# Kernel tuning notes

Measured on AMD Instinct MI355X. Metric: run time of the kernel, lower is better.

## Reference

```python
import jax, jax.numpy as jnp
import numpy as np

BN_EPS = 1e-5
CLUSTER_SIZE = 32  # K (real clusters kept after softmax)


def setup_inputs() -> dict:
    key = jax.random.key(0)
    ks = jax.random.split(key, 7)
    B, N, D, Ktot, K = 4096, 128, 512, 48, 32
    x = jax.random.normal(ks[0], (B, N, D), dtype=jnp.float32)
    clusters = jax.random.normal(ks[1], (D, Ktot), dtype=jnp.float32) / np.sqrt(D)
    bn_w = jax.random.uniform(ks[2], (Ktot,), dtype=jnp.float32)
    bn_b = jax.random.normal(ks[3], (Ktot,), dtype=jnp.float32)
    bn_rm = jax.random.normal(ks[4], (Ktot,), dtype=jnp.float32)
    bn_rv = jax.random.uniform(ks[5], (Ktot,), dtype=jnp.float32)  # positive variance
    clusters2 = jax.random.normal(ks[6], (1, D, K), dtype=jnp.float32) / np.sqrt(D)
    return {"x": x, "clusters": clusters, "bn_w": bn_w, "bn_b": bn_b,
            "bn_rm": bn_rm, "bn_rv": bn_rv, "clusters2": clusters2}


def reference(x, clusters, bn_w, bn_b, bn_rm, bn_rv, clusters2):
    # x: [B, N, D]; clusters: [D, Ktot]; clusters2: [1, D, K]
    B, N, D = x.shape
    K = clusters2.shape[-1]
    # cluster projection: [B, N, Ktot]
    logits = jnp.einsum('bnd,dk->bnk', x, clusters)
    # inference BatchNorm1d (affine with running stats)
    inv_std = jax.lax.rsqrt(bn_rv + BN_EPS)
    logits = (logits - bn_rm) * inv_std * bn_w + bn_b
    # softmax over real + ghost clusters, then drop ghost (no renorm)
    assignment = jax.nn.softmax(logits, axis=-1)[..., :K]  # [B, N, K]
    a_sum = jnp.sum(assignment, axis=1, keepdims=True)      # [B, 1, K]
    a = a_sum * clusters2                                   # [B, D, K]
    # weighted VLAD accumulate: [B, D, K]
    vlad = jnp.einsum('bnk,bnd->bdk', assignment, x) - a
    # intra-normalize (L2 across descriptor dim D, per cluster)
    vlad = vlad / jnp.maximum(jnp.linalg.norm(vlad, axis=1, keepdims=True), 1e-12)
    # flatten and L2-normalize full vector
    vlad = vlad.reshape(B, D * K)
    vlad = vlad / jnp.maximum(jnp.linalg.norm(vlad, axis=1, keepdims=True), 1e-12)
    return vlad
```

## Files before the change

### kernel.cpp

```cpp
#include <hip/hip_runtime.h>

typedef unsigned short u16;
typedef unsigned int u32;
typedef __attribute__((ext_vector_type(8))) short short8;
typedef __attribute__((ext_vector_type(4))) float f32x4;
typedef __attribute__((ext_vector_type(4))) u32 u32x4;

#define NPT 128
#define DIM 512
#define KT 48
#define KC 32
#define BPB 16

__device__ __forceinline__ u16 f2bf(float f) {
    unsigned u = __builtin_bit_cast(unsigned, f);
    return (u16)((u + 0x7FFFu + ((u >> 16) & 1u)) >> 16);
}

__device__ __forceinline__ u32 cvtpk(float lo, float hi) {
    u32 r;
    asm("v_cvt_pk_bf16_f32 %0, %1, %2" : "=v"(r) : "v"(lo), "v"(hi));
    return r;
}

__device__ __forceinline__ void lds_barrier() {
    asm volatile("s_waitcnt lgkmcnt(0)" ::: "memory");
    __builtin_amdgcn_s_barrier();
}

__device__ __forceinline__ int swz(int n) {
    return ((n & 7) ^ (((n >> 3) & 1) << 2)) << 4;
}

__global__ void prep_kernel(const float* __restrict__ clusters,
                            const float* __restrict__ bn_w,
                            const float* __restrict__ bn_b,
                            const float* __restrict__ bn_rm,
                            const float* __restrict__ bn_rv,
                            u16* __restrict__ cTs,
                            float* __restrict__ tvec) {
    const int k = blockIdx.x;
    const float s = bn_w[k] * rsqrtf(bn_rv[k] + 1e-5f);
    if (threadIdx.x == 0) tvec[k] = bn_b[k] - bn_rm[k] * s;
    for (int d = threadIdx.x; d < DIM; d += blockDim.x)
        cTs[k * DIM + d] = f2bf(clusters[d * KT + k] * s);
}

__global__ __launch_bounds__(512)
void vlad_kernel(const float* __restrict__ x,
                 const float* __restrict__ c2,
                 const u16* __restrict__ cTs,
                 const float* __restrict__ tvec,
                 float* __restrict__ out) {
    __shared__ __align__(16) u16 cTsL[KT * DIM];
    __shared__ __align__(16) u16 buf[2][16 * DIM];
    __shared__ __align__(16) u16 aT[KC][136];
    __shared__ float asum_part[8][KC];
    __shared__ float colsq_part[8][KC];

    const int tid  = threadIdx.x;
    const int wave = tid >> 6;
    const int lane = tid & 63;
    const int lr   = lane & 15;
    const int lg   = lane >> 4;

    const int b0i = blockIdx.x * BPB;
    const float* xblk = x + (size_t)b0i * (NPT * DIM);

    const float t0 = tvec[lr], t1 = tvec[16 + lr], t2 = tvec[32 + lr];

    const int srow = tid >> 5;
    const int scol = (tid & 31) * 16;
    const int sbyte = scol * 2;
    const int ssw = swz(srow);

    #pragma unroll
    for (int i = 0; i < 6; ++i) {
        int idx = tid + i * 512;
        int k = idx >> 6, slot = idx & 63;
        u32x4 v = *(const u32x4*)(cTs + k * DIM + slot * 8);
        *(u32x4*)((char*)cTsL + k * 1024 + ((slot * 16) ^ swz(k))) = v;
    }
    {
        const float* g = xblk + srow * DIM + scol;
        f32x4 a0 = *(const f32x4*)(g);
        f32x4 a1 = *(const f32x4*)(g + 4);
        f32x4 a2 = *(const f32x4*)(g + 8);
        f32x4 a3 = *(const f32x4*)(g + 12);
        u32x4 wA, wB;
        wA[0] = cvtpk(a0[0], a0[1]); wA[1] = cvtpk(a0[2], a0[3]);
        wA[2] = cvtpk(a1[0], a1[1]); wA[3] = cvtpk(a1[2], a1[3]);
        wB[0] = cvtpk(a2[0], a2[1]); wB[1] = cvtpk(a2[2], a2[3]);
        wB[2] = cvtpk(a3[0], a3[1]); wB[3] = cvtpk(a3[2], a3[3]);
        char* dst = (char*)buf[0] + srow * 1024;
        *(u32x4*)(dst + (sbyte ^ ssw)) = wA;
        *(u32x4*)(dst + ((sbyte + 16) ^ ssw)) = wB;
    }
    __syncthreads();

    for (int m = 0; m < BPB; ++m) {
        f32x4 acc0 = {0.f,0.f,0.f,0.f}, acc1 = {0.f,0.f,0.f,0.f}, acc2 = {0.f,0.f,0.f,0.f};
        short8 af2[4][4];

        #pragma unroll
        for (int ns = 0; ns < 4; ++ns) {
            #pragma unroll
            for (int h = 0; h < 2; ++h) {
                const int j = ns * 2 + h;
                const int cur = j & 1;
                const int gnext = m * 8 + j + 1;
                const bool pOK = (gnext < BPB * 8);

                f32x4 a0, a1, a2, a3;
                if (pOK) {
                    const float* g = xblk + (size_t)gnext * (16 * DIM) + srow * DIM + scol;
                    a0 = *(const f32x4*)(g);
                    a1 = *(const f32x4*)(g + 4);
                    a2 = *(const f32x4*)(g + 8);
                    a3 = *(const f32x4*)(g + 12);
                }

                if ((lane >> 5) == h) {
                    const int nb = (lg & 1) * 8;
                    #pragma unroll
                    for (int dti = 0; dti < 4; ++dti) {
                        const int dd = wave * 128 + dti * 32 + 2 * lr;
                        short8 v;
                        #pragma unroll
                        for (int jj = 0; jj < 8; ++jj) {
                            const int rr = nb + jj;
                            v[jj] = *(const short*)((const char*)buf[cur] + rr * 1024 + (dd ^ swz(rr)));
                        }
                        af2[ns][dti] = v;
                    }
                }

                if (wave == j) {
                    const char* xb = (const char*)buf[cur] + lr * 1024;
                    const int sw = swz(lr);
                    const char* c0 = (const char*)cTsL + lr * 1024;
                    const char* c1 = (const char*)cTsL + (16 + lr) * 1024;
                    const char* c2p = (const char*)cTsL + (32 + lr) * 1024;
                    const int s1 = swz(16 + lr), s2 = swz(32 + lr);
                    #pragma unroll 2
                    for (int step = 0; step < 16; ++step) {
                        const int off = step * 64 + lg * 16;
                        short8 af  = *(const short8*)(xb + (off ^ sw));
                        short8 bb0 = *(const short8*)(c0 + (off ^ sw));
                        short8 bb1 = *(const short8*)(c1 + (off ^ s1));
                        short8 bb2 = *(const short8*)(c2p + (off ^ s2));
                        acc0 = __builtin_amdgcn_mfma_f32_16x16x32_bf16(af, bb0, acc0, 0, 0, 0);
                        acc1 = __builtin_amdgcn_mfma_f32_16x16x32_bf16(af, bb1, acc1, 0, 0, 0);
                        acc2 = __builtin_amdgcn_mfma_f32_16x16x32_bf16(af, bb2, acc2, 0, 0, 0);
                    }
                }

                if (pOK) {
                    u32x4 wA, wB;
                    wA[0] = cvtpk(a0[0], a0[1]); wA[1] = cvtpk(a0[2], a0[3]);
                    wA[2] = cvtpk(a1[0], a1[1]); wA[3] = cvtpk(a1[2], a1[3]);
                    wB[0] = cvtpk(a2[0], a2[1]); wB[1] = cvtpk(a2[2], a2[3]);
                    wB[2] = cvtpk(a3[0], a3[1]); wB[3] = cvtpk(a3[2], a3[3]);
                    char* dst = (char*)buf[cur ^ 1] + srow * 1024;
                    *(u32x4*)(dst + (sbyte ^ ssw)) = wA;
                    *(u32x4*)(dst + ((sbyte + 16) ^ ssw)) = wB;
                }
                lds_barrier();
            }
        }

        {
            float a0[4], a1[4];
            #pragma unroll
            for (int r = 0; r < 4; ++r) {
                float l0 = acc0[r] + t0, l1 = acc1[r] + t1, l2 = acc2[r] + t2;
                float mx = fmaxf(fmaxf(l0, l1), l2);
                #pragma unroll
                for (int o = 1; o < 16; o <<= 1) mx = fmaxf(mx, __shfl_xor(mx, o));
                float e0 = __expf(l0 - mx), e1 = __expf(l1 - mx), e2 = __expf(l2 - mx);
                float s = e0 + e1 + e2;
                #pragma unroll
                for (int o = 1; o < 16; o <<= 1) s += __shfl_xor(s, o);
                float inv = 1.0f / s;
                a0[r] = e0 * inv; a1[r] = e1 * inv;
            }
            float p0 = 0.f, p1 = 0.f;
            #pragma unroll
            for (int r = 0; r < 4; ++r) {
                int n = wave * 16 + lg * 4 + r;
                aT[lr][n]      = f2bf(a0[r]);
                aT[16 + lr][n] = f2bf(a1[r]);
                p0 += a0[r]; p1 += a1[r];
            }
            p0 += __shfl_xor(p0, 16); p0 += __shfl_xor(p0, 32);
            p1 += __shfl_xor(p1, 16); p1 += __shfl_xor(p1, 32);
            if (lane < 16) { asum_part[wave][lane] = p0; asum_part[wave][16 + lane] = p1; }
        }
        lds_barrier();

        f32x4 vacc[4][2];
        #pragma unroll
        for (int i = 0; i < 4; ++i) {
            vacc[i][0] = (f32x4){0.f,0.f,0.f,0.f};
            vacc[i][1] = (f32x4){0.f,0.f,0.f,0.f};
        }
        #pragma unroll
        for (int ns = 0; ns < 4; ++ns) {
            short8 bf0 = *(const short8*)(&aT[lr][ns * 32 + lg * 8]);
            short8 bf1 = *(const short8*)(&aT[16 + lr][ns * 32 + lg * 8]);
            #pragma unroll
            for (int dti = 0; dti < 4; ++dti) {
                vacc[dti][0] = __builtin_amdgcn_mfma_f32_16x16x32_bf16(af2[ns][dti], bf0, vacc[dti][0], 0, 0, 0);
                vacc[dti][1] = __builtin_amdgcn_mfma_f32_16x16x32_bf16(af2[ns][dti], bf1, vacc[dti][1], 0, 0, 0);
            }
        }

        float as0 = 0.f, as1 = 0.f;
        #pragma unroll
        for (int w2 = 0; w2 < 8; ++w2) {
            as0 += asum_part[w2][lr];
            as1 += asum_part[w2][16 + lr];
        }
        float cs0 = 0.f, cs1 = 0.f;
        #pragma unroll
        for (int dti = 0; dti < 4; ++dti) {
            #pragma unroll
            for (int r = 0; r < 4; ++r) {
                int d = (wave * 4 + dti) * 16 + lg * 4 + r;
                float v0 = vacc[dti][0][r] - as0 * c2[d * KC + lr];
                float v1 = vacc[dti][1][r] - as1 * c2[d * KC + 16 + lr];
                vacc[dti][0][r] = v0; vacc[dti][1][r] = v1;
                cs0 += v0 * v0; cs1 += v1 * v1;
            }
        }
        cs0 += __shfl_xor(cs0, 16); cs0 += __shfl_xor(cs0, 32);
        cs1 += __shfl_xor(cs1, 16); cs1 += __shfl_xor(cs1, 32);
        if (lane < 16) { colsq_part[wave][lane] = cs0; colsq_part[wave][16 + lane] = cs1; }
        lds_barrier();
        float sq0 = 0.f, sq1 = 0.f;
        #pragma unroll
        for (int w2 = 0; w2 < 8; ++w2) {
            sq0 += colsq_part[w2][lr];
            sq1 += colsq_part[w2][16 + lr];
        }
        float cn0 = sqrtf(sq0), cn1 = sqrtf(sq1);
        float s10 = 1.0f / fmaxf(cn0, 1e-12f);
        float s11 = 1.0f / fmaxf(cn1, 1e-12f);
        float c10 = cn0 * s10, c11 = cn1 * s11;
        float tot = c10 * c10 + c11 * c11;
        #pragma unroll
        for (int o = 1; o < 16; o <<= 1) tot += __shfl_xor(tot, o);
        float gs = 1.0f / fmaxf(sqrtf(tot), 1e-12f);
        float sk0 = s10 * gs, sk1 = s11 * gs;
        {
            float* ob = out + (size_t)(b0i + m) * (DIM * KC);
            #pragma unroll
            for (int dti = 0; dti < 4; ++dti) {
                #pragma unroll
                for (int r = 0; r < 4; ++r) {
                    int d = (wave * 4 + dti) * 16 + lg * 4 + r;
                    ob[d * KC + lr]      = vacc[dti][0][r] * sk0;
                    ob[d * KC + 16 + lr] = vacc[dti][1][r] * sk1;
                }
            }
        }
    }
}

extern "C" void kernel_launch(void* const* d_in, const int* in_sizes, int n_in,
                              void* d_out, int out_size, void* d_ws, size_t ws_size,
                              hipStream_t stream) {
    const float* x        = (const float*)d_in[0];
    const float* clusters = (const float*)d_in[1];
    const float* bn_w     = (const float*)d_in[2];
    const float* bn_b     = (const float*)d_in[3];
    const float* bn_rm    = (const float*)d_in[4];
    const float* bn_rv    = (const float*)d_in[5];
    const float* c2       = (const float*)d_in[6];
    float* out = (float*)d_out;

    u16*   cTs  = (u16*)d_ws;
    float* tvec = (float*)((char*)d_ws + KT * DIM * sizeof(u16));

    const int B = in_sizes[0] / (NPT * DIM);

    prep_kernel<<<KT, 256, 0, stream>>>(clusters, bn_w, bn_b, bn_rm, bn_rv, cTs, tvec);
    vlad_kernel<<<B / BPB, 512, 0, stream>>>(x, c2, cTs, tvec, out);
}
```

Baseline: 368.7 us.

## Stream x chunks directly into LDS as fp32 via global_load_lds

Replaces the register-staged load, bf16 convert and LDS store of each 16-row x chunk with asynchronous global_load_lds DMA of raw fp32 into a double-buffered LDS tile. The bf16 conversion moves to the consumers: the MFMA wave converts its A fragments after reading, and the transposed fragment gather converts after reading. The aim is to take the global-to-register round trip and its VGPR pressure off the critical path. The cost is a doubled LDS footprint for the x buffers, which may reduce occupancy, plus extra conversion and scalar LDS reads per consumer.

New measurement: 395.8 us. +7.3%, slower.

```diff
diff --git a/kernel.cpp b/kernel.cpp
--- a/kernel.cpp
+++ b/kernel.cpp
@@ -11,6 +11,7 @@
 #define KT 48
 #define KC 32
 #define BPB 16
+#define NCH (BPB * 8)
 
 __device__ __forceinline__ u16 f2bf(float f) {
     unsigned u = __builtin_bit_cast(unsigned, f);
@@ -25,6 +26,11 @@
 
 __device__ __forceinline__ void lds_barrier() {
     asm volatile("s_waitcnt lgkmcnt(0)" ::: "memory");
+    __builtin_amdgcn_s_barrier();
+}
+
+__device__ __forceinline__ void chunk_barrier() {
+    asm volatile("s_waitcnt vmcnt(0) lgkmcnt(0)" ::: "memory");
     __builtin_amdgcn_s_barrier();
 }
 
@@ -46,14 +52,30 @@
         cTs[k * DIM + d] = f2bf(clusters[d * KT + k] * s);
 }
 
+#define CH_ISSUE(c)                                                          \
+    do {                                                                     \
+        const float* gc_ = xblk + (size_t)(c) * (16 * DIM);                  \
+        float* lb_ = &bufF[(c) & 1][0];                                      \
+        _Pragma("unroll")                                                    \
+        for (int i_ = 0; i_ < 4; ++i_) {                                     \
+            const int slot_ = wave * 4 + i_;                                 \
+            const int r_ = slot_ >> 1, half_ = slot_ & 1;                    \
+            const int us_ = (half_ * 64 + lane) ^ (r_ & 7);                  \
+            __builtin_amdgcn_global_load_lds(                                \
+                (const __attribute__((address_space(1))) u32*)(gc_ + r_ * DIM + us_ * 4), \
+                (__attribute__((address_space(3))) u32*)(lb_ + slot_ * 256), \
+                16, 0, 0);                                                   \
+        }                                                                    \
+    } while (0)
+
 __global__ __launch_bounds__(512)
 void vlad_kernel(const float* __restrict__ x,
                  const float* __restrict__ c2,
                  const u16* __restrict__ cTs,
                  const float* __restrict__ tvec,
                  float* __restrict__ out) {
+    __shared__ __align__(16) float bufF[2][16 * DIM];
     __shared__ __align__(16) u16 cTsL[KT * DIM];
-    __shared__ __align__(16) u16 buf[2][16 * DIM];
     __shared__ __align__(16) u16 aT[KC][136];
     __shared__ float asum_part[8][KC];
     __shared__ float colsq_part[8][KC];
@@ -68,11 +90,6 @@
     const float* xblk = x + (size_t)b0i * (NPT * DIM);
 
     const float t0 = tvec[lr], t1 = tvec[16 + lr], t2 = tvec[32 + lr];
-
-    const int srow = tid >> 5;
-    const int scol = (tid & 31) * 16;
-    const int sbyte = scol * 2;
-    const int ssw = swz(srow);
 
     #pragma unroll
     for (int i = 0; i < 6; ++i) {
@@ -81,22 +98,7 @@
         u32x4 v = *(const u32x4*)(cTs + k * DIM + slot * 8);
         *(u32x4*)((char*)cTsL + k * 1024 + ((slot * 16) ^ swz(k))) = v;
     }
-    {
-        const float* g = xblk + srow * DIM + scol;
-        f32x4 a0 = *(const f32x4*)(g);
-        f32x4 a1 = *(const f32x4*)(g + 4);
-        f32x4 a2 = *(const f32x4*)(g + 8);
-        f32x4 a3 = *(const f32x4*)(g + 12);
-        u32x4 wA, wB;
-        wA[0] = cvtpk(a0[0], a0[1]); wA[1] = cvtpk(a0[2], a0[3]);
-        wA[2] = cvtpk(a1[0], a1[1]); wA[3] = cvtpk(a1[2], a1[3]);
-        wB[0] = cvtpk(a2[0], a2[1]); wB[1] = cvtpk(a2[2], a2[3]);
-        wB[2] = cvtpk(a3[0], a3[1]); wB[3] = cvtpk(a3[2], a3[3]);
-        char* dst = (char*)buf[0] + srow * 1024;
-        *(u32x4*)(dst + (sbyte ^ ssw)) = wA;
-        *(u32x4*)(dst + ((sbyte + 16) ^ ssw)) = wB;
-    }
-    __syncthreads();
+    CH_ISSUE(0);
 
     for (int m = 0; m < BPB; ++m) {
         f32x4 acc0 = {0.f,0.f,0.f,0.f}, acc1 = {0.f,0.f,0.f,0.f}, acc2 = {0.f,0.f,0.f,0.f};
@@ -107,65 +109,57 @@
             #pragma unroll
             for (int h = 0; h < 2; ++h) {
                 const int j = ns * 2 + h;
-                const int cur = j & 1;
-                const int gnext = m * 8 + j + 1;
-                const bool pOK = (gnext < BPB * 8);
-
-                f32x4 a0, a1, a2, a3;
-                if (pOK) {
-                    const float* g = xblk + (size_t)gnext * (16 * DIM) + srow * DIM + scol;
-                    a0 = *(const f32x4*)(g);
-                    a1 = *(const f32x4*)(g + 4);
-                    a2 = *(const f32x4*)(g + 8);
-                    a3 = *(const f32x4*)(g + 12);
-                }
+                const int g = m * 8 + j;
+
+                chunk_barrier();
+                if (g + 1 < NCH) { CH_ISSUE(g + 1); }
+
+                const float* bcur = &bufF[j & 1][0];
 
                 if ((lane >> 5) == h) {
                     const int nb = (lg & 1) * 8;
                     #pragma unroll
                     for (int dti = 0; dti < 4; ++dti) {
-                        const int dd = wave * 128 + dti * 32 + 2 * lr;
-                        short8 v;
+                        const int d = wave * 64 + dti * 16 + lr;
+                        const int u = d >> 2, o = d & 3;
+                        float f[8];
                         #pragma unroll
                         for (int jj = 0; jj < 8; ++jj) {
                             const int rr = nb + jj;
-                            v[jj] = *(const short*)((const char*)buf[cur] + rr * 1024 + (dd ^ swz(rr)));
+                            f[jj] = bcur[rr * DIM + ((u ^ (rr & 7)) * 4 + o)];
                         }
-                        af2[ns][dti] = v;
+                        u32x4 w;
+                        w[0] = cvtpk(f[0], f[1]); w[1] = cvtpk(f[2], f[3]);
+                        w[2] = cvtpk(f[4], f[5]); w[3] = cvtpk(f[6], f[7]);
+                        af2[ns][dti] = __builtin_bit_cast(short8, w);
                     }
                 }
 
                 if (wave == j) {
-                    const char* xb = (const char*)buf[cur] + lr * 1024;
-                    const int sw = swz(lr);
-                    const char* c0 = (const char*)cTsL + lr * 1024;
-                    const char* c1 = (const char*)cTsL + (16 + lr) * 1024;
-                    const char* c2p = (const char*)cTsL + (32 + lr) * 1024;
-                    const int s1 = swz(16 + lr), s2 = swz(32 + lr);
-                    #pragma unroll 2
+                    const float* xrow = bcur + lr * DIM;
+                    const int xsw = lr & 7;
+                    const char* cb0 = (const char*)cTsL + lr * 1024;
+                    const char* cb1 = (const char*)cTsL + (16 + lr) * 1024;
+                    const char* cb2 = (const char*)cTsL + (32 + lr) * 1024;
+                    const int s0 = swz(lr), s1 = swz(16 + lr), s2 = swz(32 + lr);
+                    #pragma unroll 4
                     for (int step = 0; step < 16; ++step) {
+                        const int u0 = step * 8 + lg * 2;
+                        f32x4 xa = *(const f32x4*)(xrow + (u0 ^ xsw) * 4);
+                        f32x4 xb = *(const f32x4*)(xrow + ((u0 + 1) ^ xsw) * 4);
+                        u32x4 aw;
+                        aw[0] = cvtpk(xa[0], xa[1]); aw[1] = cvtpk(xa[2], xa[3]);
+                        aw[2] = cvtpk(xb[0], xb[1]); aw[3] = cvtpk(xb[2], xb[3]);
+                        short8 af = __builtin_bit_cast(short8, aw);
                         const int off = step * 64 + lg * 16;
-                        short8 af  = *(const short8*)(xb + (off ^ sw));
-                        short8 bb0 = *(const short8*)(c0 + (off ^ sw));
-                        short8 bb1 = *(const short8*)(c1 + (off ^ s1));
-                        short8 bb2 = *(const short8*)(c2p + (off ^ s2));
+                        short8 bb0 = *(const short8*)(cb0 + (off ^ s0));
+                        short8 bb1 = *(const short8*)(cb1 + (off ^ s1));
+                        short8 bb2 = *(const short8*)(cb2 + (off ^ s2));
                         acc0 = __builtin_amdgcn_mfma_f32_16x16x32_bf16(af, bb0, acc0, 0, 0, 0);
                         acc1 = __builtin_amdgcn_mfma_f32_16x16x32_bf16(af, bb1, acc1, 0, 0, 0);
                         acc2 = __builtin_amdgcn_mfma_f32_16x16x32_bf16(af, bb2, acc2, 0, 0, 0);
                     }
                 }
-
-                if (pOK) {
-                    u32x4 wA, wB;
-                    wA[0] = cvtpk(a0[0], a0[1]); wA[1] = cvtpk(a0[2], a0[3]);
-                    wA[2] = cvtpk(a1[0], a1[1]); wA[3] = cvtpk(a1[2], a1[3]);
-                    wB[0] = cvtpk(a2[0], a2[1]); wB[1] = cvtpk(a2[2], a2[3]);
-                    wB[2] = cvtpk(a3[0], a3[1]); wB[3] = cvtpk(a3[2], a3[3]);
-                    char* dst = (char*)buf[cur ^ 1] + srow * 1024;
-                    *(u32x4*)(dst + (sbyte ^ ssw)) = wA;
-                    *(u32x4*)(dst + ((sbyte + 16) ^ ssw)) = wB;
-                }
-                lds_barrier();
             }
         }
 
```

## Drop LDS cluster staging, interleave softmax and VLAD MFMAs, raise occupancy

Applied to the files above, without the earlier changes.

Removes the 48KB shared-memory copy of the scaled cluster matrix and reads the B operand directly from global memory (cache). The softmax and assignment write now happen inside each wave's logits stage, and the VLAD MFMA for each 32-point slice runs incrementally as slices complete. This cuts af2 register storage from 16 to 4 fragments. Batches per block are halved and launch bounds request 4 waves per SIMD, aiming for higher occupancy. In exchange the cluster operands come from global memory every step, and the smaller batch count doubles the per-block setup and prologue cost.

New measurement: 1.048 ms. 2.84x slower.

```diff
diff --git a/kernel.cpp b/kernel.cpp
--- a/kernel.cpp
+++ b/kernel.cpp
@@ -10,7 +10,7 @@
 #define DIM 512
 #define KT 48
 #define KC 32
-#define BPB 16
+#define BPB 8
 
 __device__ __forceinline__ u16 f2bf(float f) {
     unsigned u = __builtin_bit_cast(unsigned, f);
@@ -46,13 +46,12 @@
         cTs[k * DIM + d] = f2bf(clusters[d * KT + k] * s);
 }
 
-__global__ __launch_bounds__(512)
+__global__ __launch_bounds__(512, 4)
 void vlad_kernel(const float* __restrict__ x,
                  const float* __restrict__ c2,
                  const u16* __restrict__ cTs,
                  const float* __restrict__ tvec,
                  float* __restrict__ out) {
-    __shared__ __align__(16) u16 cTsL[KT * DIM];
     __shared__ __align__(16) u16 buf[2][16 * DIM];
     __shared__ __align__(16) u16 aT[KC][136];
     __shared__ float asum_part[8][KC];
@@ -74,13 +73,6 @@
     const int sbyte = scol * 2;
     const int ssw = swz(srow);
 
-    #pragma unroll
-    for (int i = 0; i < 6; ++i) {
-        int idx = tid + i * 512;
-        int k = idx >> 6, slot = idx & 63;
-        u32x4 v = *(const u32x4*)(cTs + k * DIM + slot * 8);
-        *(u32x4*)((char*)cTsL + k * 1024 + ((slot * 16) ^ swz(k))) = v;
-    }
     {
         const float* g = xblk + srow * DIM + scol;
         f32x4 a0 = *(const f32x4*)(g);
@@ -99,119 +91,118 @@
     __syncthreads();
 
     for (int m = 0; m < BPB; ++m) {
-        f32x4 acc0 = {0.f,0.f,0.f,0.f}, acc1 = {0.f,0.f,0.f,0.f}, acc2 = {0.f,0.f,0.f,0.f};
-        short8 af2[4][4];
-
-        #pragma unroll
-        for (int ns = 0; ns < 4; ++ns) {
-            #pragma unroll
-            for (int h = 0; h < 2; ++h) {
-                const int j = ns * 2 + h;
-                const int cur = j & 1;
-                const int gnext = m * 8 + j + 1;
-                const bool pOK = (gnext < BPB * 8);
-
-                f32x4 a0, a1, a2, a3;
-                if (pOK) {
-                    const float* g = xblk + (size_t)gnext * (16 * DIM) + srow * DIM + scol;
-                    a0 = *(const f32x4*)(g);
-                    a1 = *(const f32x4*)(g + 4);
-                    a2 = *(const f32x4*)(g + 8);
-                    a3 = *(const f32x4*)(g + 12);
-                }
-
-                if ((lane >> 5) == h) {
-                    const int nb = (lg & 1) * 8;
-                    #pragma unroll
-                    for (int dti = 0; dti < 4; ++dti) {
-                        const int dd = wave * 128 + dti * 32 + 2 * lr;
-                        short8 v;
-                        #pragma unroll
-                        for (int jj = 0; jj < 8; ++jj) {
-                            const int rr = nb + jj;
-                            v[jj] = *(const short*)((const char*)buf[cur] + rr * 1024 + (dd ^ swz(rr)));
-                        }
-                        af2[ns][dti] = v;
-                    }
-                }
-
-                if (wave == j) {
-                    const char* xb = (const char*)buf[cur] + lr * 1024;
-                    const int sw = swz(lr);
-                    const char* c0 = (const char*)cTsL + lr * 1024;
-                    const char* c1 = (const char*)cTsL + (16 + lr) * 1024;
-                    const char* c2p = (const char*)cTsL + (32 + lr) * 1024;
-                    const int s1 = swz(16 + lr), s2 = swz(32 + lr);
-                    #pragma unroll 2
-                    for (int step = 0; step < 16; ++step) {
-                        const int off = step * 64 + lg * 16;
-                        short8 af  = *(const short8*)(xb + (off ^ sw));
-                        short8 bb0 = *(const short8*)(c0 + (off ^ sw));
-                        short8 bb1 = *(const short8*)(c1 + (off ^ s1));
-                        short8 bb2 = *(const short8*)(c2p + (off ^ s2));
-                        acc0 = __builtin_amdgcn_mfma_f32_16x16x32_bf16(af, bb0, acc0, 0, 0, 0);
-                        acc1 = __builtin_amdgcn_mfma_f32_16x16x32_bf16(af, bb1, acc1, 0, 0, 0);
-                        acc2 = __builtin_amdgcn_mfma_f32_16x16x32_bf16(af, bb2, acc2, 0, 0, 0);
-                    }
-                }
-
-                if (pOK) {
-                    u32x4 wA, wB;
-                    wA[0] = cvtpk(a0[0], a0[1]); wA[1] = cvtpk(a0[2], a0[3]);
-                    wA[2] = cvtpk(a1[0], a1[1]); wA[3] = cvtpk(a1[2], a1[3]);
-                    wB[0] = cvtpk(a2[0], a2[1]); wB[1] = cvtpk(a2[2], a2[3]);
-                    wB[2] = cvtpk(a3[0], a3[1]); wB[3] = cvtpk(a3[2], a3[3]);
-                    char* dst = (char*)buf[cur ^ 1] + srow * 1024;
-                    *(u32x4*)(dst + (sbyte ^ ssw)) = wA;
-                    *(u32x4*)(dst + ((sbyte + 16) ^ ssw)) = wB;
-                }
-                lds_barrier();
-            }
-        }
-
-        {
-            float a0[4], a1[4];
-            #pragma unroll
-            for (int r = 0; r < 4; ++r) {
-                float l0 = acc0[r] + t0, l1 = acc1[r] + t1, l2 = acc2[r] + t2;
-                float mx = fmaxf(fmaxf(l0, l1), l2);
-                #pragma unroll
-                for (int o = 1; o < 16; o <<= 1) mx = fmaxf(mx, __shfl_xor(mx, o));
-                float e0 = __expf(l0 - mx), e1 = __expf(l1 - mx), e2 = __expf(l2 - mx);
-                float s = e0 + e1 + e2;
-                #pragma unroll
-                for (int o = 1; o < 16; o <<= 1) s += __shfl_xor(s, o);
-                float inv = 1.0f / s;
-                a0[r] = e0 * inv; a1[r] = e1 * inv;
-            }
-            float p0 = 0.f, p1 = 0.f;
-            #pragma unroll
-            for (int r = 0; r < 4; ++r) {
-                int n = wave * 16 + lg * 4 + r;
-                aT[lr][n]      = f2bf(a0[r]);
-                aT[16 + lr][n] = f2bf(a1[r]);
-                p0 += a0[r]; p1 += a1[r];
-            }
-            p0 += __shfl_xor(p0, 16); p0 += __shfl_xor(p0, 32);
-            p1 += __shfl_xor(p1, 16); p1 += __shfl_xor(p1, 32);
-            if (lane < 16) { asum_part[wave][lane] = p0; asum_part[wave][16 + lane] = p1; }
-        }
-        lds_barrier();
-
+        short8 af2[4];
         f32x4 vacc[4][2];
         #pragma unroll
         for (int i = 0; i < 4; ++i) {
             vacc[i][0] = (f32x4){0.f,0.f,0.f,0.f};
             vacc[i][1] = (f32x4){0.f,0.f,0.f,0.f};
         }
-        #pragma unroll
-        for (int ns = 0; ns < 4; ++ns) {
-            short8 bf0 = *(const short8*)(&aT[lr][ns * 32 + lg * 8]);
-            short8 bf1 = *(const short8*)(&aT[16 + lr][ns * 32 + lg * 8]);
+
+        #pragma unroll
+        for (int j = 0; j < 8; ++j) {
+            const int g = m * 8 + j;
+            const int cur = j & 1;
+            const bool pOK = (g + 1 < BPB * 8);
+
+            f32x4 a0, a1, a2, a3;
+            if (pOK) {
+                const float* gl = xblk + (size_t)(g + 1) * (16 * DIM) + srow * DIM + scol;
+                a0 = *(const f32x4*)(gl);
+                a1 = *(const f32x4*)(gl + 4);
+                a2 = *(const f32x4*)(gl + 8);
+                a3 = *(const f32x4*)(gl + 12);
+            }
+
+            if ((j & 1) == 0 && j >= 2) {
+                const int p = (j >> 1) - 1;
+                short8 bf0 = *(const short8*)(&aT[lr][p * 32 + lg * 8]);
+                short8 bf1 = *(const short8*)(&aT[16 + lr][p * 32 + lg * 8]);
+                #pragma unroll
+                for (int dti = 0; dti < 4; ++dti) {
+                    vacc[dti][0] = __builtin_amdgcn_mfma_f32_16x16x32_bf16(af2[dti], bf0, vacc[dti][0], 0, 0, 0);
+                    vacc[dti][1] = __builtin_amdgcn_mfma_f32_16x16x32_bf16(af2[dti], bf1, vacc[dti][1], 0, 0, 0);
+                }
+            }
+
+            if ((lg >> 1) == cur) {
+                const int nb = (lg & 1) * 8;
+                #pragma unroll
+                for (int dti = 0; dti < 4; ++dti) {
+                    const int dd = wave * 128 + dti * 32 + 2 * lr;
+                    short8 v;
+                    #pragma unroll
+                    for (int jj = 0; jj < 8; ++jj) {
+                        const int rr = nb + jj;
+                        v[jj] = *(const short*)((const char*)buf[cur] + rr * 1024 + (dd ^ swz(rr)));
+                    }
+                    af2[dti] = v;
+                }
+            }
+
+            if (wave == j) {
+                f32x4 acc0 = {0.f,0.f,0.f,0.f}, acc1 = {0.f,0.f,0.f,0.f}, acc2 = {0.f,0.f,0.f,0.f};
+                const char* xb = (const char*)buf[cur] + lr * 1024;
+                const int sw = swz(lr);
+                #pragma unroll 2
+                for (int step = 0; step < 16; ++step) {
+                    const int d0 = step * 32 + lg * 8;
+                    const int off = step * 64 + lg * 16;
+                    short8 af  = *(const short8*)(xb + (off ^ sw));
+                    short8 bb0 = *(const short8*)(cTs + (0 * 16 + lr) * DIM + d0);
+                    short8 bb1 = *(const short8*)(cTs + (1 * 16 + lr) * DIM + d0);
+                    short8 bb2 = *(const short8*)(cTs + (2 * 16 + lr) * DIM + d0);
+                    acc0 = __builtin_amdgcn_mfma_f32_16x16x32_bf16(af, bb0, acc0, 0, 0, 0);
+                    acc1 = __builtin_amdgcn_mfma_f32_16x16x32_bf16(af, bb1, acc1, 0, 0, 0);
+                    acc2 = __builtin_amdgcn_mfma_f32_16x16x32_bf16(af, bb2, acc2, 0, 0, 0);
+                }
+                float sa0[4], sa1[4];
+                #pragma unroll
+                for (int r = 0; r < 4; ++r) {
+                    float l0 = acc0[r] + t0, l1 = acc1[r] + t1, l2 = acc2[r] + t2;
+                    float mx = fmaxf(fmaxf(l0, l1), l2);
+                    #pragma unroll
+                    for (int o = 1; o < 16; o <<= 1) mx = fmaxf(mx, __shfl_xor(mx, o));
+                    float e0 = __expf(l0 - mx), e1 = __expf(l1 - mx), e2 = __expf(l2 - mx);
+                    float s = e0 + e1 + e2;
+                    #pragma unroll
+                    for (int o = 1; o < 16; o <<= 1) s += __shfl_xor(s, o);
+                    float inv = 1.0f / s;
+                    sa0[r] = e0 * inv; sa1[r] = e1 * inv;
+                }
+                float p0 = 0.f, p1 = 0.f;
+                #pragma unroll
+                for (int r = 0; r < 4; ++r) {
+                    int n = j * 16 + lg * 4 + r;
+                    aT[lr][n]      = f2bf(sa0[r]);
+                    aT[16 + lr][n] = f2bf(sa1[r]);
+                    p0 += sa0[r]; p1 += sa1[r];
+                }
+                p0 += __shfl_xor(p0, 16); p0 += __shfl_xor(p0, 32);
+                p1 += __shfl_xor(p1, 16); p1 += __shfl_xor(p1, 32);
+                if (lane < 16) { asum_part[j][lane] = p0; asum_part[j][16 + lane] = p1; }
+            }
+
+            if (pOK) {
+                u32x4 wA, wB;
+                wA[0] = cvtpk(a0[0], a0[1]); wA[1] = cvtpk(a0[2], a0[3]);
+                wA[2] = cvtpk(a1[0], a1[1]); wA[3] = cvtpk(a1[2], a1[3]);
+                wB[0] = cvtpk(a2[0], a2[1]); wB[1] = cvtpk(a2[2], a2[3]);
+                wB[2] = cvtpk(a3[0], a3[1]); wB[3] = cvtpk(a3[2], a3[3]);
+                char* dst = (char*)buf[cur ^ 1] + srow * 1024;
+                *(u32x4*)(dst + (sbyte ^ ssw)) = wA;
+                *(u32x4*)(dst + ((sbyte + 16) ^ ssw)) = wB;
+            }
+            lds_barrier();
+        }
+
+        {
+            short8 bf0 = *(const short8*)(&aT[lr][3 * 32 + lg * 8]);
+            short8 bf1 = *(const short8*)(&aT[16 + lr][3 * 32 + lg * 8]);
             #pragma unroll
             for (int dti = 0; dti < 4; ++dti) {
-                vacc[dti][0] = __builtin_amdgcn_mfma_f32_16x16x32_bf16(af2[ns][dti], bf0, vacc[dti][0], 0, 0, 0);
-                vacc[dti][1] = __builtin_amdgcn_mfma_f32_16x16x32_bf16(af2[ns][dti], bf1, vacc[dti][1], 0, 0, 0);
+                vacc[dti][0] = __builtin_amdgcn_mfma_f32_16x16x32_bf16(af2[dti], bf0, vacc[dti][0], 0, 0, 0);
+                vacc[dti][1] = __builtin_amdgcn_mfma_f32_16x16x32_bf16(af2[dti], bf1, vacc[dti][1], 0, 0, 0);
             }
         }
 
```
